# Kernel optimization log

Measured on AMD Instinct MI355X. Metric: run time of the kernel, lower is better.

## Reference

```python
import jax, jax.numpy as jnp
import numpy as np

NEG_SLOPE = 0.2
LN_EPS = 1e-6

B, L, D, H = 32, 512, 256, 4
N = B * L
E = 65536
C = D  # per-head out channels (GATConv out_channels=d_model)


def setup_inputs() -> dict:
    key = jax.random.key(0)
    ks = jax.random.split(key, 10)
    s = 1.0 / np.sqrt(D)
    inputs = jax.random.normal(ks[0], (B, L, D), dtype=jnp.float32)
    edge_index = jax.random.randint(ks[1], (2, E), 0, N, dtype=jnp.int64)
    return {
        "inputs": inputs,
        "edge_index": edge_index,
        "ln_gamma": jnp.ones((D,), jnp.float32),
        "ln_beta": jnp.zeros((D,), jnp.float32),
        "W1": jax.random.normal(ks[2], (D, D), jnp.float32) * s,   # linear_before_gnn
        "b1": jnp.zeros((D,), jnp.float32),
        "W_gat": jax.random.normal(ks[3], (H * C, D), jnp.float32) * s,  # GATConv.lin (no bias)
        "att_src": jax.random.normal(ks[4], (H, C), jnp.float32) * s,
        "att_dst": jax.random.normal(ks[5], (H, C), jnp.float32) * s,
        "bias_gat": jnp.zeros((C,), jnp.float32),  # concat=False -> size out_channels
        "W2": jax.random.normal(ks[6], (D, D), jnp.float32) * s,   # linear_after_gnn
        "b2": jnp.zeros((D,), jnp.float32),
    }


def _gat_conv(x, edge_index, W_gat, att_src, att_dst, bias_gat):
    # x: [N, D] -> project to [N, H, C]
    xh = (x @ W_gat.T).reshape(N, H, C)
    # add self loops (PyG default add_self_loops=True)
    loops = jnp.arange(N, dtype=edge_index.dtype)
    src = jnp.concatenate([edge_index[0], loops])  # message source j
    dst = jnp.concatenate([edge_index[1], loops])  # message target i
    # per-node attention logits [N, H]
    a_src = jnp.einsum("nhc,hc->nh", xh, att_src)
    a_dst = jnp.einsum("nhc,hc->nh", xh, att_dst)
    # per-edge logits and segment softmax over destination node
    e = jax.nn.leaky_relu(a_src[src] + a_dst[dst], NEG_SLOPE)  # [Etot, H]
    e_max = jax.ops.segment_max(e, dst, num_segments=N)        # every node has a self loop
    e = jnp.exp(e - e_max[dst])
    denom = jax.ops.segment_sum(e, dst, num_segments=N)
    alpha = e / denom[dst]                                     # [Etot, H]
    # weighted message aggregation (dropout on alpha skipped: eval mode)
    msg = xh[src] * alpha[:, :, None]                          # [Etot, H, C]
    out = jax.ops.segment_sum(msg, dst, num_segments=N)        # [N, H, C]
    return out.mean(axis=1) + bias_gat                         # concat=False -> head mean


def reference(inputs, edge_index, ln_gamma, ln_beta, W1, b1, W_gat, att_src, att_dst, bias_gat, W2, b2):
    # LayerNorm(eps=1e-6)
    mu = inputs.mean(-1, keepdims=True)
    var = jnp.mean((inputs - mu) ** 2, axis=-1, keepdims=True)
    x = (inputs - mu) * jax.lax.rsqrt(var + LN_EPS) * ln_gamma + ln_beta
    x = x.reshape(-1, D)
    gnn_in = x @ W1.T + b1
    gnn_out = _gat_conv(gnn_in, edge_index, W_gat, att_src, att_dst, bias_gat)
    y = gnn_out @ W2.T + b2
    # dropout is identity in eval mode; residual add
    return y.reshape(B, L, D) + inputs
```

## Files before the change

### kernel.cpp

```cpp
#include <hip/hip_runtime.h>
#include <math.h>

#define N_NODES 16384
#define D_MODEL 256
#define H_HEADS 4
#define C_CH 256
#define E_EDGES 65536
#define ETOT (E_EDGES + N_NODES)
#define HC 1024

typedef __bf16 bf16x8 __attribute__((ext_vector_type(8)));
typedef __bf16 bf16x4 __attribute__((ext_vector_type(4)));
typedef float f32x4 __attribute__((ext_vector_type(4)));

__device__ __forceinline__ __bf16 f2bf(float f) { return (__bf16)f; }
__device__ __forceinline__ float bf2f(__bf16 b) { return (float)b; }

__global__ __launch_bounds__(256) void prep1_ln(
    const float* __restrict__ Wg, const float* __restrict__ att_src,
    const float* __restrict__ att_dst, const float* __restrict__ W2,
    const int* __restrict__ ei, const float* __restrict__ in,
    const float* __restrict__ gamma, const float* __restrict__ beta,
    float* __restrict__ t, float* __restrict__ V, int* __restrict__ deg,
    __bf16* __restrict__ x_ln)
{
    int b = blockIdx.x;
    int tid = threadIdx.x;
    if (b >= 1408) {
        int wave = tid >> 6, lane = tid & 63;
        int row = (b - 1408) * 4 + wave;
        float4 v = ((const float4*)(in + (size_t)row * D_MODEL))[lane];
        float s  = v.x + v.y + v.z + v.w;
        float sq = v.x*v.x + v.y*v.y + v.z*v.z + v.w*v.w;
        for (int off = 32; off; off >>= 1) {
            s  += __shfl_xor(s,  off);
            sq += __shfl_xor(sq, off);
        }
        float mean = s * (1.0f / D_MODEL);
        float var  = sq * (1.0f / D_MODEL) - mean * mean;
        float inv  = rsqrtf(var + 1e-6f);
        float4 g = ((const float4*)gamma)[lane];
        float4 bb = ((const float4*)beta)[lane];
        bf16x4 o;
        o[0] = f2bf((v.x - mean) * inv * g.x + bb.x);
        o[1] = f2bf((v.y - mean) * inv * g.y + bb.y);
        o[2] = f2bf((v.z - mean) * inv * g.z + bb.z);
        o[3] = f2bf((v.w - mean) * inv * g.w + bb.w);
        *(bf16x4*)(x_ln + (size_t)row * D_MODEL + lane * 4) = o;
        return;
    }
    if (b < 64) {
        int v = b >> 3, sl = b & 7, h = v & 3;
        const float* att = ((v < 4) ? att_src : att_dst) + h * C_CH;
        float acc = 0.f;
        #pragma unroll
        for (int j = 0; j < 32; ++j) {
            int c = sl * 32 + j;
            acc = fmaf(Wg[(size_t)(h * 256 + c) * 256 + tid], att[c], acc);
        }
        atomicAdd(&t[v * 256 + tid], acc);
        return;
    }
    if (b < 1088) {
        int bb2 = b - 64;
        int orig = bb2 >> 2, cs = bb2 & 3;
        int og = (orig & 63) * 4, h = orig >> 6;
        const float* w2r = W2 + (size_t)og * 256;
        const float* wgp = Wg + ((size_t)h * 256) * 256 + tid;
        float a0 = 0.f, a1 = 0.f, a2 = 0.f, a3 = 0.f;
        int cb = cs * 64;
        #pragma unroll 4
        for (int c = cb; c < cb + 64; ++c) {
            float wv = wgp[(size_t)c * 256];
            a0 = fmaf(w2r[c],       wv, a0);
            a1 = fmaf(w2r[256 + c], wv, a1);
            a2 = fmaf(w2r[512 + c], wv, a2);
            a3 = fmaf(w2r[768 + c], wv, a3);
        }
        size_t base = (size_t)og * 1024 + h * 256 + tid;
        atomicAdd(&V[base],        a0);
        atomicAdd(&V[base + 1024], a1);
        atomicAdd(&V[base + 2048], a2);
        atomicAdd(&V[base + 3072], a3);
        return;
    }
    {
        int e = (b - 1088) * 256 + tid;
        int dst = (e < E_EDGES) ? ei[E_EDGES + e] : (e - E_EDGES);
        atomicAdd(deg + dst, 1);
    }
}

__global__ __launch_bounds__(256) void prep2(
    const float* __restrict__ t, const float* __restrict__ W1,
    const float* __restrict__ b1, const float* __restrict__ V,
    const float* __restrict__ W2, const float* __restrict__ bg,
    const float* __restrict__ b2, float* __restrict__ u2,
    float* __restrict__ c0, float* __restrict__ Wzf,
    float* __restrict__ bias_z, const int* __restrict__ deg,
    int* __restrict__ row_st)
{
    __shared__ float red[4][4];
    __shared__ int wsum[4];
    int b = blockIdx.x;
    int d = threadIdx.x;

    if (b < 1024) {
        int orig = b >> 2, ks = b & 3;
        int og = (orig & 63) * 4, h = orig >> 6;
        int lane = d & 63, wid = d >> 6;
        const float* vr = V + (size_t)og * 1024 + h * 256;
        float a0 = 0.f, a1 = 0.f, a2 = 0.f, a3 = 0.f;
        int kb = ks * 64;
        #pragma unroll 4
        for (int k = kb; k < kb + 64; ++k) {
            float w1v = W1[(size_t)k * 256 + d];
            a0 = fmaf(vr[k],        w1v, a0);
            a1 = fmaf(vr[1024 + k], w1v, a1);
            a2 = fmaf(vr[2048 + k], w1v, a2);
            a3 = fmaf(vr[3072 + k], w1v, a3);
        }
        size_t base = (size_t)og * 1024 + h * 256 + d;
        atomicAdd(&Wzf[base],        a0);
        atomicAdd(&Wzf[base + 1024], a1);
        atomicAdd(&Wzf[base + 2048], a2);
        atomicAdd(&Wzf[base + 3072], a3);

        if (ks == 0) {
            float b1v = b1[d];
            #pragma unroll
            for (int j = 0; j < 4; ++j) {
                float p = vr[(size_t)j * 1024 + d] * b1v;
                for (int s = 32; s; s >>= 1) p += __shfl_xor(p, s);
                if (lane == 0) red[j][wid] = p;
            }
            __syncthreads();
            if (d < 4) {
                float s = red[d][0] + red[d][1] + red[d][2] + red[d][3];
                atomicAdd(&bias_z[og + d], 0.25f * s);
            }
            if (h == 0) {
                __syncthreads();
                float bgv = bg[d];
                #pragma unroll
                for (int j = 0; j < 4; ++j) {
                    float q = W2[(size_t)(og + j) * 256 + d] * bgv;
                    for (int s = 32; s; s >>= 1) q += __shfl_xor(q, s);
                    if (lane == 0) red[j][wid] = q;
                }
                __syncthreads();
                if (d < 4) {
                    float s = red[d][0] + red[d][1] + red[d][2] + red[d][3];
                    atomicAdd(&bias_z[og + d], s + b2[og + d]);
                }
            }
        }
        return;
    }
    if (b < 1088) {
        int bb = b - 1024;
        int v = bb >> 3, sl = bb & 7;
        const float* tv = t + v * 256;
        float acc = 0.f;
        #pragma unroll
        for (int j = 0; j < 32; ++j) {
            int k = sl * 32 + j;
            acc = fmaf(tv[k], W1[(size_t)k * 256 + d], acc);
        }
        atomicAdd(&u2[v * 256 + d], acc);
        if (d < 32) {
            float p = tv[sl * 32 + d] * b1[sl * 32 + d];
            for (int s = 16; s; s >>= 1) p += __shfl_xor(p, s);
            if (d == 0) atomicAdd(&c0[v], p);
        }
        return;
    }
    {
        int lane = d & 63, wid = d >> 6;
        int base = d * 64;
        int4 dv[16];
        #pragma unroll
        for (int j = 0; j < 16; ++j) dv[j] = ((const int4*)(deg + base))[j];
        int run = 0;
        #pragma unroll
        for (int j = 0; j < 16; ++j)
            run += dv[j].x + dv[j].y + dv[j].z + dv[j].w;
        int x = run;
        #pragma unroll
        for (int off = 1; off < 64; off <<= 1) {
            int y = __shfl_up(x, off);
            if (lane >= off) x += y;
        }
        if (lane == 63) wsum[wid] = x;
        __syncthreads();
        int woff = 0;
        #pragma unroll
        for (int wdx = 0; wdx < 4; ++wdx)
            if (wdx < wid) woff += wsum[wdx];
        int excl = woff + x - run;
        int r2v = 0;
        #pragma unroll
        for (int j = 0; j < 16; ++j) {
            int4 w;
            w.x = excl + r2v; r2v += dv[j].x;
            w.y = excl + r2v; r2v += dv[j].y;
            w.z = excl + r2v; r2v += dv[j].z;
            w.w = excl + r2v; r2v += dv[j].w;
            ((int4*)(row_st + base))[j] = w;
        }
        if (d == 255) row_st[N_NODES] = excl + r2v;
    }
}

__global__ __launch_bounds__(256) void logits_scatter_cvt(
    const __bf16* __restrict__ x_ln, const float* __restrict__ u2,
    const float* __restrict__ c0, float* __restrict__ a_src,
    float* __restrict__ a_dst, const int* __restrict__ ei,
    const int* __restrict__ row_st, int* __restrict__ cnt,
    int* __restrict__ csr_src, const float* __restrict__ Wzf,
    __bf16* __restrict__ Wz)
{
    int b = blockIdx.x;
    int tid = threadIdx.x;
    if (b >= 4416) {
        int idx = (b - 4416) * 256 + tid;
        float4 v = ((const float4*)Wzf)[idx];
        bf16x4 o;
        o[0] = f2bf(v.x); o[1] = f2bf(v.y); o[2] = f2bf(v.z); o[3] = f2bf(v.w);
        *(bf16x4*)(Wz + (size_t)idx * 4) = o;
        return;
    }
    if (b >= 4096) {
        int e = (b - 4096) * 256 + tid;
        int src, dst;
        if (e < E_EDGES) { src = ei[e]; dst = ei[E_EDGES + e]; }
        else             { src = dst = e - E_EDGES; }
        int pos = atomicAdd(cnt + dst, 1);
        csr_src[row_st[dst] + pos] = src;
        return;
    }
    __shared__ float u2s[8][256];
    __shared__ float c0s[8];
    #pragma unroll
    for (int k = 0; k < 8; ++k) u2s[k][tid] = u2[k * 256 + tid];
    if (tid < 8) c0s[tid] = c0[tid];
    __syncthreads();

    int wave = tid >> 6, lane = tid & 63;
    int n = b * 4 + wave;
    int v = lane >> 3, p = lane & 7;
    const __bf16* xp = x_ln + (size_t)n * D_MODEL + p * 32;
    const float*  up = &u2s[v][p * 32];
    float acc = 0.f;
    #pragma unroll
    for (int ti = 0; ti < 4; ++ti) {
        bf16x8 x = *(const bf16x8*)(xp + ti * 8);
        #pragma unroll
        for (int j = 0; j < 8; ++j)
            acc = fmaf(bf2f(x[j]), up[ti * 8 + j], acc);
    }
    acc += __shfl_xor(acc, 1);
    acc += __shfl_xor(acc, 2);
    acc += __shfl_xor(acc, 4);
    if (p == 0) {
        float o = acc + c0s[v];
        if (v < 4) a_src[n * H_HEADS + v] = o;
        else       a_dst[n * H_HEADS + (v - 4)] = o;
    }
}

__global__ __launch_bounds__(256) void gat_fused(
    const __bf16* __restrict__ x_ln, const float* __restrict__ a_src,
    const float* __restrict__ a_dst, const int* __restrict__ row_start,
    const int* __restrict__ csr_src, __bf16* __restrict__ agg)
{
    int wave = threadIdx.x >> 6, lane = threadIdx.x & 63;
    int i = blockIdx.x * 4 + wave;
    int rs = row_start[i], deg = row_start[i + 1] - rs;
    float4 ad = *(const float4*)(a_dst + i * H_HEADS);

    float acc[4][4] = {};
    float sm0 = 0.f, sm1 = 0.f, sm2 = 0.f, sm3 = 0.f;
    int e = 0;
    for (; e + 2 <= deg; e += 2) {
        int s0 = csr_src[rs + e];
        int s1 = csr_src[rs + e + 1];
        float4 as0 = *(const float4*)(a_src + s0 * H_HEADS);
        float4 as1 = *(const float4*)(a_src + s1 * H_HEADS);
        bf16x4 x0 = *(const bf16x4*)(x_ln + (size_t)s0 * D_MODEL + lane * 4);
        bf16x4 x1 = *(const bf16x4*)(x_ln + (size_t)s1 * D_MODEL + lane * 4);
        float l00 = as0.x + ad.x, l01 = as0.y + ad.y,
              l02 = as0.z + ad.z, l03 = as0.w + ad.w;
        float l10 = as1.x + ad.x, l11 = as1.y + ad.y,
              l12 = as1.z + ad.z, l13 = as1.w + ad.w;
        l00 = (l00 > 0.f) ? l00 : 0.2f * l00;
        l01 = (l01 > 0.f) ? l01 : 0.2f * l01;
        l02 = (l02 > 0.f) ? l02 : 0.2f * l02;
        l03 = (l03 > 0.f) ? l03 : 0.2f * l03;
        l10 = (l10 > 0.f) ? l10 : 0.2f * l10;
        l11 = (l11 > 0.f) ? l11 : 0.2f * l11;
        l12 = (l12 > 0.f) ? l12 : 0.2f * l12;
        l13 = (l13 > 0.f) ? l13 : 0.2f * l13;
        float w00 = __expf(l00), w01 = __expf(l01),
              w02 = __expf(l02), w03 = __expf(l03);
        float w10 = __expf(l10), w11 = __expf(l11),
              w12 = __expf(l12), w13 = __expf(l13);
        sm0 += w00 + w10; sm1 += w01 + w11;
        sm2 += w02 + w12; sm3 += w03 + w13;
        #pragma unroll
        for (int j = 0; j < 4; ++j) {
            float xv0 = bf2f(x0[j]);
            float xv1 = bf2f(x1[j]);
            acc[0][j] = fmaf(w00, xv0, acc[0][j]);
            acc[1][j] = fmaf(w01, xv0, acc[1][j]);
            acc[2][j] = fmaf(w02, xv0, acc[2][j]);
            acc[3][j] = fmaf(w03, xv0, acc[3][j]);
            acc[0][j] = fmaf(w10, xv1, acc[0][j]);
            acc[1][j] = fmaf(w11, xv1, acc[1][j]);
            acc[2][j] = fmaf(w12, xv1, acc[2][j]);
            acc[3][j] = fmaf(w13, xv1, acc[3][j]);
        }
    }
    if (e < deg) {
        int s = csr_src[rs + e];
        float4 as = *(const float4*)(a_src + s * H_HEADS);
        bf16x4 x = *(const bf16x4*)(x_ln + (size_t)s * D_MODEL + lane * 4);
        float l0 = as.x + ad.x, l1 = as.y + ad.y,
              l2 = as.z + ad.z, l3 = as.w + ad.w;
        l0 = (l0 > 0.f) ? l0 : 0.2f * l0;
        l1 = (l1 > 0.f) ? l1 : 0.2f * l1;
        l2 = (l2 > 0.f) ? l2 : 0.2f * l2;
        l3 = (l3 > 0.f) ? l3 : 0.2f * l3;
        float w0 = __expf(l0), w1 = __expf(l1);
        float w2 = __expf(l2), w3 = __expf(l3);
        sm0 += w0; sm1 += w1; sm2 += w2; sm3 += w3;
        #pragma unroll
        for (int j = 0; j < 4; ++j) {
            float xv = bf2f(x[j]);
            acc[0][j] = fmaf(w0, xv, acc[0][j]);
            acc[1][j] = fmaf(w1, xv, acc[1][j]);
            acc[2][j] = fmaf(w2, xv, acc[2][j]);
            acc[3][j] = fmaf(w3, xv, acc[3][j]);
        }
    }
    float sc[4] = {0.25f / sm0, 0.25f / sm1, 0.25f / sm2, 0.25f / sm3};
    #pragma unroll
    for (int h = 0; h < 4; ++h) {
        bf16x4 o;
        #pragma unroll
        for (int j = 0; j < 4; ++j) o[j] = f2bf(acc[h][j] * sc[h]);
        *(bf16x4*)(agg + (size_t)i * HC + h * 256 + lane * 4) = o;
    }
}

#define APAD 72

__global__ __launch_bounds__(256) void gemm_skinny(
    const __bf16* __restrict__ A, const __bf16* __restrict__ B,
    const float* __restrict__ bias, const float* __restrict__ resid,
    float* __restrict__ outf, int K)
{
    __shared__ __align__(16) __bf16 As[64 * APAD];
    __shared__ __align__(16) __bf16 Bs[256 * APAD];
    int tid  = threadIdx.x;
    int lane = tid & 63;
    int w    = tid >> 6;
    int quad = lane >> 4;
    int l16  = lane & 15;
    int m0 = blockIdx.x * 64;
    int n0 = w * 64;

    int srow = tid >> 3, sp = tid & 7;
    const __bf16* Ab = A + (size_t)(m0 + srow) * K + sp * 8;
    const __bf16* Bb = B + (size_t)srow * K + sp * 8;
    size_t rstride = (size_t)32 * K;

    f32x4 acc[4][4] = {};

    bf16x8 a0_0, a0_1, b0_[8];
    bf16x8 a1_0, a1_1, b1_[8];

    auto compute = [&]() {
        #pragma unroll
        for (int ks = 0; ks < 2; ++ks) {
            bf16x8 af[4], bfr[4];
            #pragma unroll
            for (int mt = 0; mt < 4; ++mt)
                af[mt] = *(const bf16x8*)(As + (mt * 16 + l16) * APAD
                                          + ks * 32 + quad * 8);
            #pragma unroll
            for (int nt = 0; nt < 4; ++nt)
                bfr[nt] = *(const bf16x8*)(Bs + (n0 + nt * 16 + l16) * APAD
                                           + ks * 32 + quad * 8);
            #pragma unroll
            for (int mt = 0; mt < 4; ++mt)
                #pragma unroll
                for (int nt = 0; nt < 4; ++nt)
                    acc[mt][nt] = __builtin_amdgcn_mfma_f32_16x16x32_bf16(
                        af[mt], bfr[nt], acc[mt][nt], 0, 0, 0);
        }
    };

    a0_0 = *(const bf16x8*)(Ab);
    a0_1 = *(const bf16x8*)(Ab + rstride);
    #pragma unroll
    for (int t = 0; t < 8; ++t)
        b0_[t] = *(const bf16x8*)(Bb + t * rstride);

    for (int kb = 0; kb < K; kb += 128) {
        {
            const __bf16* Ap = Ab + kb + 64;
            const __bf16* Bp = Bb + kb + 64;
            a1_0 = *(const bf16x8*)(Ap);
            a1_1 = *(const bf16x8*)(Ap + rstride);
            #pragma unroll
            for (int t = 0; t < 8; ++t)
                b1_[t] = *(const bf16x8*)(Bp + t * rstride);
        }
        __syncthreads();
        *(bf16x8*)(As + srow * APAD + sp * 8)        = a0_0;
        *(bf16x8*)(As + (srow + 32) * APAD + sp * 8) = a0_1;
        #pragma unroll
        for (int t = 0; t < 8; ++t)
            *(bf16x8*)(Bs + (srow + t * 32) * APAD + sp * 8) = b0_[t];
        __syncthreads();
        compute();

        if (kb + 128 < K) {
            const __bf16* Ap = Ab + kb + 128;
            const __bf16* Bp = Bb + kb + 128;
            a0_0 = *(const bf16x8*)(Ap);
            a0_1 = *(const bf16x8*)(Ap + rstride);
            #pragma unroll
            for (int t = 0; t < 8; ++t)
                b0_[t] = *(const bf16x8*)(Bp + t * rstride);
        }
        __syncthreads();
        *(bf16x8*)(As + srow * APAD + sp * 8)        = a1_0;
        *(bf16x8*)(As + (srow + 32) * APAD + sp * 8) = a1_1;
        #pragma unroll
        for (int t = 0; t < 8; ++t)
            *(bf16x8*)(Bs + (srow + t * 32) * APAD + sp * 8) = b1_[t];
        __syncthreads();
        compute();
    }

    #pragma unroll
    for (int nt = 0; nt < 4; ++nt) {
        int col = n0 + nt * 16 + l16;
        float bv = bias[col];
        #pragma unroll
        for (int mt = 0; mt < 4; ++mt) {
            int row = m0 + mt * 16 + quad * 4;
            #pragma unroll
            for (int r = 0; r < 4; ++r) {
                size_t off = (size_t)(row + r) * C_CH + col;
                outf[off] = acc[mt][nt][r] + bv + resid[off];
            }
        }
    }
}

extern "C" void kernel_launch(void* const* d_in, const int* in_sizes, int n_in,
                              void* d_out, int out_size, void* d_ws, size_t ws_size,
                              hipStream_t stream)
{
    const float* inp      = (const float*)d_in[0];
    const int*   ei       = (const int*)  d_in[1];
    const float* ln_gamma = (const float*)d_in[2];
    const float* ln_beta  = (const float*)d_in[3];
    const float* W1       = (const float*)d_in[4];
    const float* b1       = (const float*)d_in[5];
    const float* W_gat    = (const float*)d_in[6];
    const float* att_src  = (const float*)d_in[7];
    const float* att_dst  = (const float*)d_in[8];
    const float* bias_gat = (const float*)d_in[9];
    const float* W2       = (const float*)d_in[10];
    const float* b2       = (const float*)d_in[11];

    char* ws = (char*)d_ws;
    __bf16* x_ln_bf = (__bf16*)(ws);
    __bf16* agg_bf  = (__bf16*)(ws + (8ull  << 20));
    __bf16* Wz_b    = (__bf16*)(ws + (40ull << 20));
    float*  a_src_b = (float*)(ws + (41ull << 20));
    float*  a_dst_b = a_src_b + (size_t)N_NODES * H_HEADS;
    float*  t_vec   = (float*)(ws + (42ull << 20));
    float*  u2      = t_vec + 2048;
    float*  c0      = u2 + 2048;
    float*  bias_z  = c0 + 8;
    int*    deg     = (int*)(bias_z + 256);
    int*    cnt     = deg + N_NODES;
    float*  V_f     = (float*)(cnt + N_NODES);
    float*  Wzf     = V_f + 256 * 1024;
    int*    row_st  = (int*)(Wzf + 256 * 1024);
    int*    csr_src = row_st + N_NODES + 4;

    size_t zbytes = (2048 + 2048 + 8 + 256) * sizeof(float)
                  + 2 * N_NODES * sizeof(int)
                  + 2 * 256 * 1024 * sizeof(float);
    hipMemsetAsync(t_vec, 0, zbytes, stream);

    prep1_ln<<<1408 + 4096, 256, 0, stream>>>(W_gat, att_src, att_dst, W2, ei,
                                              inp, ln_gamma, ln_beta,
                                              t_vec, V_f, deg, x_ln_bf);
    prep2<<<1089, 256, 0, stream>>>(t_vec, W1, b1, V_f, W2, bias_gat, b2,
                                    u2, c0, Wzf, bias_z, deg, row_st);
    logits_scatter_cvt<<<4096 + 320 + 256, 256, 0, stream>>>(
        x_ln_bf, u2, c0, a_src_b, a_dst_b, ei, row_st, cnt, csr_src,
        Wzf, Wz_b);
    gat_fused<<<N_NODES / 4, 256, 0, stream>>>(x_ln_bf, a_src_b, a_dst_b,
                                               row_st, csr_src, agg_bf);
    gemm_skinny<<<N_NODES / 64, 256, 0, stream>>>(agg_bf, Wz_b, bias_z, inp,
                                                  (float*)d_out, HC);
}
```

Measured before the change: 165.2 us.

## Replace CSR prefix-scan with fixed-capacity per-node adjacency slots

Builds the destination adjacency directly in prep1 into fixed slots of 64 per node using atomic counters, which removes the degree prefix scan and the separate scatter pass in the logits kernel. In gat_fused each wave loads all neighbour indices in one coalesced read and broadcasts them with shuffles, and the edge loop is unrolled by four to keep more loads in flight. The weight-fold GEMV blocks are also split twice as finely. This assumes no node has more than 64 incoming edges, which holds for random graphs of this size but is not guaranteed in general and would overflow silently otherwise.

After: 163.6 us. No clear change (-0.9%).

```diff
diff --git a/kernel.cpp b/kernel.cpp
--- a/kernel.cpp
+++ b/kernel.cpp
@@ -8,6 +8,7 @@
 #define E_EDGES 65536
 #define ETOT (E_EDGES + N_NODES)
 #define HC 1024
+#define MAXDEG 64
 
 typedef __bf16 bf16x8 __attribute__((ext_vector_type(8)));
 typedef __bf16 bf16x4 __attribute__((ext_vector_type(4)));
@@ -21,14 +22,14 @@
     const float* __restrict__ att_dst, const float* __restrict__ W2,
     const int* __restrict__ ei, const float* __restrict__ in,
     const float* __restrict__ gamma, const float* __restrict__ beta,
-    float* __restrict__ t, float* __restrict__ V, int* __restrict__ deg,
-    __bf16* __restrict__ x_ln)
+    float* __restrict__ t, float* __restrict__ V, int* __restrict__ cnt,
+    int* __restrict__ csr, __bf16* __restrict__ x_ln)
 {
     int b = blockIdx.x;
     int tid = threadIdx.x;
-    if (b >= 1408) {
+    if (b >= 2432) {
         int wave = tid >> 6, lane = tid & 63;
-        int row = (b - 1408) * 4 + wave;
+        int row = (b - 2432) * 4 + wave;
         float4 v = ((const float4*)(in + (size_t)row * D_MODEL))[lane];
         float s  = v.x + v.y + v.z + v.w;
         float sq = v.x*v.x + v.y*v.y + v.z*v.z + v.w*v.w;
@@ -61,16 +62,16 @@
         atomicAdd(&t[v * 256 + tid], acc);
         return;
     }
-    if (b < 1088) {
+    if (b < 2112) {
         int bb2 = b - 64;
-        int orig = bb2 >> 2, cs = bb2 & 3;
+        int orig = bb2 >> 3, cs = bb2 & 7;
         int og = (orig & 63) * 4, h = orig >> 6;
         const float* w2r = W2 + (size_t)og * 256;
         const float* wgp = Wg + ((size_t)h * 256) * 256 + tid;
         float a0 = 0.f, a1 = 0.f, a2 = 0.f, a3 = 0.f;
-        int cb = cs * 64;
+        int cb = cs * 32;
         #pragma unroll 4
-        for (int c = cb; c < cb + 64; ++c) {
+        for (int c = cb; c < cb + 32; ++c) {
             float wv = wgp[(size_t)c * 256];
             a0 = fmaf(w2r[c],       wv, a0);
             a1 = fmaf(w2r[256 + c], wv, a1);
@@ -85,9 +86,12 @@
         return;
     }
     {
-        int e = (b - 1088) * 256 + tid;
-        int dst = (e < E_EDGES) ? ei[E_EDGES + e] : (e - E_EDGES);
-        atomicAdd(deg + dst, 1);
+        int e = (b - 2112) * 256 + tid;
+        int src, dst;
+        if (e < E_EDGES) { src = ei[e]; dst = ei[E_EDGES + e]; }
+        else             { src = dst = e - E_EDGES; }
+        int pos = atomicAdd(cnt + dst, 1);
+        csr[(size_t)dst * MAXDEG + pos] = src;
     }
 }
 
@@ -97,23 +101,21 @@
     const float* __restrict__ W2, const float* __restrict__ bg,
     const float* __restrict__ b2, float* __restrict__ u2,
     float* __restrict__ c0, float* __restrict__ Wzf,
-    float* __restrict__ bias_z, const int* __restrict__ deg,
-    int* __restrict__ row_st)
+    float* __restrict__ bias_z)
 {
     __shared__ float red[4][4];
-    __shared__ int wsum[4];
     int b = blockIdx.x;
     int d = threadIdx.x;
 
-    if (b < 1024) {
-        int orig = b >> 2, ks = b & 3;
+    if (b < 2048) {
+        int orig = b >> 3, ks = b & 7;
         int og = (orig & 63) * 4, h = orig >> 6;
         int lane = d & 63, wid = d >> 6;
         const float* vr = V + (size_t)og * 1024 + h * 256;
         float a0 = 0.f, a1 = 0.f, a2 = 0.f, a3 = 0.f;
-        int kb = ks * 64;
+        int kb = ks * 32;
         #pragma unroll 4
-        for (int k = kb; k < kb + 64; ++k) {
+        for (int k = kb; k < kb + 32; ++k) {
             float w1v = W1[(size_t)k * 256 + d];
             a0 = fmaf(vr[k],        w1v, a0);
             a1 = fmaf(vr[1024 + k], w1v, a1);
@@ -157,8 +159,8 @@
         }
         return;
     }
-    if (b < 1088) {
-        int bb = b - 1024;
+    {
+        int bb = b - 2048;
         int v = bb >> 3, sl = bb & 7;
         const float* tv = t + v * 256;
         float acc = 0.f;
@@ -173,70 +175,23 @@
             for (int s = 16; s; s >>= 1) p += __shfl_xor(p, s);
             if (d == 0) atomicAdd(&c0[v], p);
         }
-        return;
-    }
-    {
-        int lane = d & 63, wid = d >> 6;
-        int base = d * 64;
-        int4 dv[16];
-        #pragma unroll
-        for (int j = 0; j < 16; ++j) dv[j] = ((const int4*)(deg + base))[j];
-        int run = 0;
-        #pragma unroll
-        for (int j = 0; j < 16; ++j)
-            run += dv[j].x + dv[j].y + dv[j].z + dv[j].w;
-        int x = run;
-        #pragma unroll
-        for (int off = 1; off < 64; off <<= 1) {
-            int y = __shfl_up(x, off);
-            if (lane >= off) x += y;
-        }
-        if (lane == 63) wsum[wid] = x;
-        __syncthreads();
-        int woff = 0;
-        #pragma unroll
-        for (int wdx = 0; wdx < 4; ++wdx)
-            if (wdx < wid) woff += wsum[wdx];
-        int excl = woff + x - run;
-        int r2v = 0;
-        #pragma unroll
-        for (int j = 0; j < 16; ++j) {
-            int4 w;
-            w.x = excl + r2v; r2v += dv[j].x;
-            w.y = excl + r2v; r2v += dv[j].y;
-            w.z = excl + r2v; r2v += dv[j].z;
-            w.w = excl + r2v; r2v += dv[j].w;
-            ((int4*)(row_st + base))[j] = w;
-        }
-        if (d == 255) row_st[N_NODES] = excl + r2v;
-    }
-}
-
-__global__ __launch_bounds__(256) void logits_scatter_cvt(
+    }
+}
+
+__global__ __launch_bounds__(256) void logits_cvt(
     const __bf16* __restrict__ x_ln, const float* __restrict__ u2,
     const float* __restrict__ c0, float* __restrict__ a_src,
-    float* __restrict__ a_dst, const int* __restrict__ ei,
-    const int* __restrict__ row_st, int* __restrict__ cnt,
-    int* __restrict__ csr_src, const float* __restrict__ Wzf,
+    float* __restrict__ a_dst, const float* __restrict__ Wzf,
     __bf16* __restrict__ Wz)
 {
     int b = blockIdx.x;
     int tid = threadIdx.x;
-    if (b >= 4416) {
-        int idx = (b - 4416) * 256 + tid;
+    if (b >= 4096) {
+        int idx = (b - 4096) * 256 + tid;
         float4 v = ((const float4*)Wzf)[idx];
         bf16x4 o;
         o[0] = f2bf(v.x); o[1] = f2bf(v.y); o[2] = f2bf(v.z); o[3] = f2bf(v.w);
         *(bf16x4*)(Wz + (size_t)idx * 4) = o;
-        return;
-    }
-    if (b >= 4096) {
-        int e = (b - 4096) * 256 + tid;
-        int src, dst;
-        if (e < E_EDGES) { src = ei[e]; dst = ei[E_EDGES + e]; }
-        else             { src = dst = e - E_EDGES; }
-        int pos = atomicAdd(cnt + dst, 1);
-        csr_src[row_st[dst] + pos] = src;
         return;
     }
     __shared__ float u2s[8][256];
@@ -271,58 +226,68 @@
 
 __global__ __launch_bounds__(256) void gat_fused(
     const __bf16* __restrict__ x_ln, const float* __restrict__ a_src,
-    const float* __restrict__ a_dst, const int* __restrict__ row_start,
-    const int* __restrict__ csr_src, __bf16* __restrict__ agg)
+    const float* __restrict__ a_dst, const int* __restrict__ cnt,
+    const int* __restrict__ csr, __bf16* __restrict__ agg)
 {
     int wave = threadIdx.x >> 6, lane = threadIdx.x & 63;
     int i = blockIdx.x * 4 + wave;
-    int rs = row_start[i], deg = row_start[i + 1] - rs;
+    int deg = cnt[i];
+    int sidx = csr[(size_t)i * MAXDEG + lane];
     float4 ad = *(const float4*)(a_dst + i * H_HEADS);
 
     float acc[4][4] = {};
     float sm0 = 0.f, sm1 = 0.f, sm2 = 0.f, sm3 = 0.f;
+
     int e = 0;
-    for (; e + 2 <= deg; e += 2) {
-        int s0 = csr_src[rs + e];
-        int s1 = csr_src[rs + e + 1];
-        float4 as0 = *(const float4*)(a_src + s0 * H_HEADS);
-        float4 as1 = *(const float4*)(a_src + s1 * H_HEADS);
-        bf16x4 x0 = *(const bf16x4*)(x_ln + (size_t)s0 * D_MODEL + lane * 4);
-        bf16x4 x1 = *(const bf16x4*)(x_ln + (size_t)s1 * D_MODEL + lane * 4);
-        float l00 = as0.x + ad.x, l01 = as0.y + ad.y,
-              l02 = as0.z + ad.z, l03 = as0.w + ad.w;
-        float l10 = as1.x + ad.x, l11 = as1.y + ad.y,
-              l12 = as1.z + ad.z, l13 = as1.w + ad.w;
-        l00 = (l00 > 0.f) ? l00 : 0.2f * l00;
-        l01 = (l01 > 0.f) ? l01 : 0.2f * l01;
-        l02 = (l02 > 0.f) ? l02 : 0.2f * l02;
-        l03 = (l03 > 0.f) ? l03 : 0.2f * l03;
-        l10 = (l10 > 0.f) ? l10 : 0.2f * l10;
-        l11 = (l11 > 0.f) ? l11 : 0.2f * l11;
-        l12 = (l12 > 0.f) ? l12 : 0.2f * l12;
-        l13 = (l13 > 0.f) ? l13 : 0.2f * l13;
-        float w00 = __expf(l00), w01 = __expf(l01),
-              w02 = __expf(l02), w03 = __expf(l03);
-        float w10 = __expf(l10), w11 = __expf(l11),
-              w12 = __expf(l12), w13 = __expf(l13);
-        sm0 += w00 + w10; sm1 += w01 + w11;
-        sm2 += w02 + w12; sm3 += w03 + w13;
+    for (; e + 4 <= deg; e += 4) {
+        int s0 = __shfl(sidx, e);
+        int s1 = __shfl(sidx, e + 1);
+        int s2 = __shfl(sidx, e + 2);
+        int s3 = __shfl(sidx, e + 3);
+        float4 A0 = *(const float4*)(a_src + s0 * H_HEADS);
+        float4 A1 = *(const float4*)(a_src + s1 * H_HEADS);
+        float4 A2 = *(const float4*)(a_src + s2 * H_HEADS);
+        float4 A3 = *(const float4*)(a_src + s3 * H_HEADS);
+        bf16x4 X0 = *(const bf16x4*)(x_ln + (size_t)s0 * D_MODEL + lane * 4);
+        bf16x4 X1 = *(const bf16x4*)(x_ln + (size_t)s1 * D_MODEL + lane * 4);
+        bf16x4 X2 = *(const bf16x4*)(x_ln + (size_t)s2 * D_MODEL + lane * 4);
+        bf16x4 X3 = *(const bf16x4*)(x_ln + (size_t)s3 * D_MODEL + lane * 4);
+
+        float l[4][4] = {
+            {A0.x + ad.x, A0.y + ad.y, A0.z + ad.z, A0.w + ad.w},
+            {A1.x + ad.x, A1.y + ad.y, A1.z + ad.z, A1.w + ad.w},
+            {A2.x + ad.x, A2.y + ad.y, A2.z + ad.z, A2.w + ad.w},
+            {A3.x + ad.x, A3.y + ad.y, A3.z + ad.z, A3.w + ad.w}};
+        float wgt[4][4];
+        #pragma unroll
+        for (int q = 0; q < 4; ++q)
+            #pragma unroll
+            for (int h = 0; h < 4; ++h) {
+                float lv = l[q][h];
+                lv = (lv > 0.f) ? lv : 0.2f * lv;
+                wgt[q][h] = __expf(lv);
+            }
+        sm0 += wgt[0][0] + wgt[1][0] + wgt[2][0] + wgt[3][0];
+        sm1 += wgt[0][1] + wgt[1][1] + wgt[2][1] + wgt[3][1];
+        sm2 += wgt[0][2] + wgt[1][2] + wgt[2][2] + wgt[3][2];
+        sm3 += wgt[0][3] + wgt[1][3] + wgt[2][3] + wgt[3][3];
         #pragma unroll
         for (int j = 0; j < 4; ++j) {
-            float xv0 = bf2f(x0[j]);
-            float xv1 = bf2f(x1[j]);
-            acc[0][j] = fmaf(w00, xv0, acc[0][j]);
-            acc[1][j] = fmaf(w01, xv0, acc[1][j]);
-            acc[2][j] = fmaf(w02, xv0, acc[2][j]);
-            acc[3][j] = fmaf(w03, xv0, acc[3][j]);
-            acc[0][j] = fmaf(w10, xv1, acc[0][j]);
-            acc[1][j] = fmaf(w11, xv1, acc[1][j]);
-            acc[2][j] = fmaf(w12, xv1, acc[2][j]);
-            acc[3][j] = fmaf(w13, xv1, acc[3][j]);
-        }
-    }
-    if (e < deg) {
-        int s = csr_src[rs + e];
+            float x0 = bf2f(X0[j]), x1 = bf2f(X1[j]);
+            float x2 = bf2f(X2[j]), x3 = bf2f(X3[j]);
+            #pragma unroll
+            for (int h = 0; h < 4; ++h) {
+                float a = acc[h][j];
+                a = fmaf(wgt[0][h], x0, a);
+                a = fmaf(wgt[1][h], x1, a);
+                a = fmaf(wgt[2][h], x2, a);
+                a = fmaf(wgt[3][h], x3, a);
+                acc[h][j] = a;
+            }
+        }
+    }
+    for (; e < deg; ++e) {
+        int s = __shfl(sidx, e);
         float4 as = *(const float4*)(a_src + s * H_HEADS);
         bf16x4 x = *(const bf16x4*)(x_ln + (size_t)s * D_MODEL + lane * 4);
         float l0 = as.x + ad.x, l1 = as.y + ad.y,
@@ -488,28 +453,25 @@
     float*  u2      = t_vec + 2048;
     float*  c0      = u2 + 2048;
     float*  bias_z  = c0 + 8;
-    int*    deg     = (int*)(bias_z + 256);
-    int*    cnt     = deg + N_NODES;
+    int*    cnt     = (int*)(bias_z + 256);
     float*  V_f     = (float*)(cnt + N_NODES);
     float*  Wzf     = V_f + 256 * 1024;
-    int*    row_st  = (int*)(Wzf + 256 * 1024);
-    int*    csr_src = row_st + N_NODES + 4;
+    int*    csr     = (int*)(ws + (45ull << 20));
 
     size_t zbytes = (2048 + 2048 + 8 + 256) * sizeof(float)
-                  + 2 * N_NODES * sizeof(int)
+                  + N_NODES * sizeof(int)
                   + 2 * 256 * 1024 * sizeof(float);
     hipMemsetAsync(t_vec, 0, zbytes, stream);
 
-    prep1_ln<<<1408 + 4096, 256, 0, stream>>>(W_gat, att_src, att_dst, W2, ei,
+    prep1_ln<<<2432 + 4096, 256, 0, stream>>>(W_gat, att_src, att_dst, W2, ei,
                                               inp, ln_gamma, ln_beta,
-                                              t_vec, V_f, deg, x_ln_bf);
-    prep2<<<1089, 256, 0, stream>>>(t_vec, W1, b1, V_f, W2, bias_gat, b2,
-                                    u2, c0, Wzf, bias_z, deg, row_st);
-    logits_scatter_cvt<<<4096 + 320 + 256, 256, 0, stream>>>(
-        x_ln_bf, u2, c0, a_src_b, a_dst_b, ei, row_st, cnt, csr_src,
-        Wzf, Wz_b);
+                                              t_vec, V_f, cnt, csr, x_ln_bf);
+    prep2<<<2112, 256, 0, stream>>>(t_vec, W1, b1, V_f, W2, bias_gat, b2,
+                                    u2, c0, Wzf, bias_z);
+    logits_cvt<<<4096 + 256, 256, 0, stream>>>(x_ln_bf, u2, c0,
+                                               a_src_b, a_dst_b, Wzf, Wz_b);
     gat_fused<<<N_NODES / 4, 256, 0, stream>>>(x_ln_bf, a_src_b, a_dst_b,
-                                               row_st, csr_src, agg_bf);
+                                               cnt, csr, agg_bf);
     gemm_skinny<<<N_NODES / 64, 256, 0, stream>>>(agg_bf, Wz_b, bias_z, inp,
                                                   (float*)d_out, HC);
 }
```
